# Performance work log

Measured on AMD Instinct MI355X. Metric: run time of the kernel, lower is better.

Reference implementation:

```python
import jax, jax.numpy as jnp
import numpy as np

B, S, D, E, K, NS = 4, 1024, 1024, 8, 2, 2
H = 4 * D
TEMP = 0.1
SCALE = 0.02


def setup_inputs() -> dict:
    key = jax.random.key(0)
    ks = jax.random.split(key, 12)
    f32 = jnp.float32
    return {
        "x": jax.random.normal(ks[0], (B, S, D), f32),
        "Ws1": jax.random.normal(ks[1], (NS, D, H), f32) * SCALE,
        "bs1": jnp.zeros((NS, H), f32),
        "Ws2": jax.random.normal(ks[2], (NS, H, D), f32) * SCALE,
        "bs2": jnp.zeros((NS, D), f32),
        "We1": jax.random.normal(ks[3], (E, D, H), f32) * SCALE,
        "be1": jnp.zeros((E, H), f32),
        "We2": jax.random.normal(ks[4], (E, H, D), f32) * SCALE,
        "be2": jnp.zeros((E, D), f32),
        "Wr": jax.random.normal(ks[5], (D, E), f32) * SCALE,
        "br": jnp.zeros((E,), f32),
        "gumbel": jax.random.gumbel(ks[6], (B, S, E), f32),
    }


def reference(x, Ws1, bs1, Ws2, bs2, We1, be1, We2, be2, Wr, br, gumbel):
    act = jax.nn.gelu
    # shared experts: dense FFN per shared expert, summed over experts
    hs = act(jnp.einsum('bsd,edh->ebsh', x, Ws1) + bs1[:, None, None, :])
    shared_sum = (jnp.einsum('ebsh,ehd->ebsd', hs, Ws2)
                  + bs2[:, None, None, :]).sum(axis=0)  # [B,S,D]
    # routing experts: ALL experts computed densely over all tokens
    he = act(jnp.einsum('bsd,edh->ebsh', x, We1) + be1[:, None, None, :])
    all_experts = jnp.einsum('ebsh,ehd->ebsd', he, We2) + be2[:, None, None, :]  # [E,B,S,D]
    # router + gumbel-softmax top-k selection
    logits = x @ Wr + br                                  # [B,S,E]
    router_probs = jax.nn.softmax((logits + gumbel) / TEMP, axis=-1)
    chosen = jax.lax.top_k(router_probs, K)[1]            # [B,S,K] int
    one_hot = jax.nn.one_hot(chosen, E, dtype=x.dtype)    # [B,S,K,E]
    # unweighted sum of selected experts' outputs (sum over k and experts)
    out = jnp.einsum('bske,ebsd->bsd', one_hot, all_experts)
    return out + shared_sum
```

## Files before the change

kernel.cpp:

```cpp
#include <hip/hip_runtime.h>
#include <cstdint>
#include <cstddef>

#define T_TOK 4096
#define DDIM 1024
#define HDIM 4096
#define NEXP 8
#define NSHARED 2
#define RT_CAP 9216

typedef unsigned short ushort_t;
typedef __attribute__((ext_vector_type(8))) short short8;
typedef __attribute__((ext_vector_type(4))) float f32x4;

__device__ inline ushort_t f2bf(float f) {
  unsigned u = __float_as_uint(f);
  u += 0x7fffu + ((u >> 16) & 1u);
  return (ushort_t)(u >> 16);
}

__device__ inline void async_copy16(const ushort_t* g, ushort_t* l) {
  __builtin_amdgcn_global_load_lds(
      (const __attribute__((address_space(1))) void*)g,
      (__attribute__((address_space(3))) void*)l, 16, 0, 0);
}

__device__ inline float gelu_tanh(float x) {
  float u = 0.7978845608028654f * (x + 0.044715f * x * x * x);
  float th = 1.0f - 2.0f / (__expf(2.0f * u) + 1.0f);
  return 0.5f * x * (1.0f + th);
}

__device__ inline void swizzle_xy(int* bx, int* by) {
  int l = blockIdx.x + gridDim.x * blockIdx.y;
  int g = l >> 8;
  *bx = (l & 7) + (g << 3);
  *by = (l >> 3) & 31;
}

__global__ __launch_bounds__(256) void router_kernel(
    const float* __restrict__ x, const float* __restrict__ Wr,
    const float* __restrict__ br, const float* __restrict__ gum,
    int* __restrict__ choice, int* __restrict__ cnt) {
  int lane = threadIdx.x & 63;
  int wv = blockIdx.x * 4 + (threadIdx.x >> 6);
  if (wv >= T_TOK) return;
  const float* xr = x + (long)wv * DDIM;
  float acc[NEXP] = {0.f, 0.f, 0.f, 0.f, 0.f, 0.f, 0.f, 0.f};
  for (int d = lane; d < DDIM; d += 64) {
    float xv = xr[d];
    const float* w = Wr + d * NEXP;
#pragma unroll
    for (int e = 0; e < NEXP; e++) acc[e] += xv * w[e];
  }
#pragma unroll
  for (int e = 0; e < NEXP; e++) {
    float v = acc[e];
#pragma unroll
    for (int o = 32; o > 0; o >>= 1) v += __shfl_down(v, o);
    acc[e] = v;
  }
  if (lane == 0) {
    float vals[NEXP];
#pragma unroll
    for (int e = 0; e < NEXP; e++) vals[e] = acc[e] + br[e] + gum[(long)wv * NEXP + e];
    int i1 = 0; float b1 = vals[0];
#pragma unroll
    for (int e = 1; e < NEXP; e++) if (vals[e] > b1) { b1 = vals[e]; i1 = e; }
    int i2 = -1; float b2 = -3.4e38f;
#pragma unroll
    for (int e = 0; e < NEXP; e++) if (e != i1 && vals[e] > b2) { b2 = vals[e]; i2 = e; }
    choice[wv] = i1 | (i2 << 4);
    atomicAdd(&cnt[i1], 1);
    atomicAdd(&cnt[i2], 1);
  }
}

__global__ void prefix_kernel(const int* __restrict__ cnt, int* __restrict__ base,
                              int* __restrict__ fill) {
  if (threadIdx.x == 0 && blockIdx.x == 0) {
    int off = 0;
    for (int e = 0; e < NEXP; e++) {
      base[e] = off;
      off += (cnt[e] + 127) & ~127;
      fill[e] = 0;
    }
  }
}

__global__ __launch_bounds__(256) void scatter_kernel(
    const int* __restrict__ choice, const int* __restrict__ base,
    int* __restrict__ fill, int* __restrict__ idx, int* __restrict__ pos) {
  int t = blockIdx.x * 256 + threadIdx.x;
  if (t >= T_TOK) return;
  int c = choice[t];
  int e1 = c & 15, e2 = (c >> 4) & 15;
  int p1 = base[e1] + atomicAdd(&fill[e1], 1);
  idx[p1] = t; pos[2 * t] = p1;
  int p2 = base[e2] + atomicAdd(&fill[e2], 1);
  idx[p2] = t; pos[2 * t + 1] = p2;
}

__global__ __launch_bounds__(256) void cast_x_kernel(
    const float* __restrict__ in, ushort_t* __restrict__ out, int n4) {
  int i = blockIdx.x * 256 + threadIdx.x;
  if (i >= n4) return;
  float4 v = ((const float4*)in)[i];
  ushort4 o = make_ushort4(f2bf(v.x), f2bf(v.y), f2bf(v.z), f2bf(v.w));
  ((ushort4*)out)[i] = o;
}

__global__ __launch_bounds__(256) void transpose_cast10(
    const float* __restrict__ inS, const float* __restrict__ inE,
    ushort_t* __restrict__ out, int R, int C) {
  __shared__ float tile[32][33];
  int z = blockIdx.z;
  const float* in = (z < NSHARED) ? inS + (size_t)z * R * C
                                  : inE + (size_t)(z - NSHARED) * R * C;
  ushort_t* op = out + (size_t)z * R * C;
  int c0 = blockIdx.x * 32, r0 = blockIdx.y * 32;
  int tx = threadIdx.x, ty = threadIdx.y;
#pragma unroll
  for (int k = 0; k < 4; k++)
    tile[ty + 8 * k][tx] = in[(long)(r0 + ty + 8 * k) * C + (c0 + tx)];
  __syncthreads();
#pragma unroll
  for (int k = 0; k < 4; k++)
    op[(long)(c0 + ty + 8 * k) * R + (r0 + tx)] = f2bf(tile[tx][ty + 8 * k]);
}

__global__ __launch_bounds__(256) void gemm1_kernel(
    const ushort_t* __restrict__ xb, const ushort_t* __restrict__ W1t,
    const float* __restrict__ bs1, const float* __restrict__ be1,
    ushort_t* __restrict__ h_sh, ushort_t* __restrict__ h_rt,
    const int* __restrict__ cnt, const int* __restrict__ base,
    const int* __restrict__ idx) {
  __shared__ ushort_t As[2 * 128 * 32];
  __shared__ ushort_t Bs[2 * 128 * 32];

  int tid = threadIdx.x;
  int z = blockIdx.z;
  int bx, by; swizzle_xy(&bx, &by);
  int row0 = by * 128, col0 = bx * 128;
  bool sh = (z < NSHARED);

  int e = 0, M = T_TOK, base_e = 0;
  const ushort_t* Bp;
  const float* bias;
  if (sh) {
    Bp = W1t + (size_t)z * HDIM * DDIM;
    bias = bs1 + (size_t)z * HDIM;
  } else {
    e = z - NSHARED; M = cnt[e];
    if (row0 >= M) return;
    base_e = base[e];
    Bp = W1t + (size_t)(NSHARED + e) * HDIM * DDIM;
    bias = be1 + (size_t)e * HDIM;
  }

  int tq = tid & 3, tr = tid >> 2;
  const ushort_t *aS, *aS2;
  if (sh) {
    aS = xb + (size_t)(row0 + tr) * DDIM + tq * 8;
    aS2 = aS + (size_t)64 * DDIM;
  } else {
    int s1 = row0 + tr;      if (s1 > M - 1) s1 = M - 1;
    int s2 = row0 + tr + 64; if (s2 > M - 1) s2 = M - 1;
    aS  = xb + (size_t)idx[base_e + s1] * DDIM + tq * 8;
    aS2 = xb + (size_t)idx[base_e + s2] * DDIM + tq * 8;
  }
  const ushort_t* bS = Bp + (size_t)(col0 + tr) * DDIM + tq * 8;
  const ushort_t* bS2 = bS + (size_t)64 * DDIM;
  ushort_t* aD = As + tid * 8;
  ushort_t* bD = Bs + tid * 8;

  int lane = tid & 63, wv = tid >> 6;
  int wr = wv >> 1, wc = wv & 1;
  int ln = lane & 15, quad = lane >> 4;
  f32x4 acc[4][4] = {};
  const ushort_t* aLds = As + (wr * 64 + ln) * 32 + quad * 8;
  const ushort_t* bLds = Bs + (wc * 64 + ln) * 32 + quad * 8;

  for (int k0 = 0; k0 < DDIM; k0 += 64) {
    async_copy16(aS, aD);             async_copy16(aS2, aD + 2048);
    async_copy16(aS + 32, aD + 4096); async_copy16(aS2 + 32, aD + 6144);
    async_copy16(bS, bD);             async_copy16(bS2, bD + 2048);
    async_copy16(bS + 32, bD + 4096); async_copy16(bS2 + 32, bD + 6144);
    __syncthreads();
#pragma unroll
    for (int s = 0; s < 2; s++) {
      short8 af[4], bf[4];
#pragma unroll
      for (int i = 0; i < 4; i++) {
        af[i] = *(const short8*)(aLds + s * 4096 + i * 16 * 32);
        bf[i] = *(const short8*)(bLds + s * 4096 + i * 16 * 32);
      }
#pragma unroll
      for (int i = 0; i < 4; i++)
#pragma unroll
        for (int j = 0; j < 4; j++)
          acc[i][j] = __builtin_amdgcn_mfma_f32_16x16x32_bf16(af[i], bf[j],
                                                              acc[i][j], 0, 0, 0);
    }
    __syncthreads();
    aS += 64; aS2 += 64; bS += 64; bS2 += 64;
  }

#pragma unroll
  for (int i = 0; i < 4; i++) {
    int rowB = row0 + wr * 64 + i * 16 + quad * 4;
#pragma unroll
    for (int j = 0; j < 4; j++) {
      int col = col0 + wc * 64 + j * 16 + ln;
      float b = bias[col];
#pragma unroll
      for (int r = 0; r < 4; r++) {
        int t = rowB + r;
        float v = gelu_tanh(acc[i][j][r] + b);
        if (sh) {
          h_sh[(size_t)t * (2 * HDIM) + (size_t)z * HDIM + col] = f2bf(v);
        } else if (t < M) {
          h_rt[((size_t)base_e + t) * HDIM + col] = f2bf(v);
        }
      }
    }
  }
}

__global__ __launch_bounds__(256) void gemm2_kernel(
    const ushort_t* __restrict__ h_sh, const ushort_t* __restrict__ h_rt,
    const ushort_t* __restrict__ W2t, float* __restrict__ outShA,
    float* __restrict__ outShB, float* __restrict__ outRt,
    const int* __restrict__ cnt, const int* __restrict__ base) {
  __shared__ ushort_t As[2 * 128 * 32];
  __shared__ ushort_t Bs[2 * 128 * 32];

  int tid = threadIdx.x;
  int z = blockIdx.z;
  int bx, by; swizzle_xy(&bx, &by);
  int row0 = by * 128, col0 = bx * 128;
  bool sh = (z < NSHARED);

  int e = 0, M = T_TOK, base_e = 0;
  const ushort_t* Ap;
  long lda;
  const ushort_t* Bp;
  float* outP;
  if (sh) {
    Ap = h_sh + (size_t)z * HDIM;
    lda = 2 * HDIM;
    Bp = W2t + (size_t)z * DDIM * HDIM;
    outP = (z == 0) ? outShA : outShB;
  } else {
    e = z - NSHARED; M = cnt[e];
    if (row0 >= M) return;
    base_e = base[e];
    Ap = h_rt + (size_t)base_e * HDIM;
    lda = HDIM;
    Bp = W2t + (size_t)(NSHARED + e) * DDIM * HDIM;
    outP = outRt + (size_t)base_e * DDIM;
  }

  int tq = tid & 3, tr = tid >> 2;
  const ushort_t* aS = Ap + (long)(row0 + tr) * lda + tq * 8;
  const ushort_t* aS2 = aS + 64L * lda;
  const ushort_t* bS = Bp + (size_t)(col0 + tr) * HDIM + tq * 8;
  const ushort_t* bS2 = bS + (size_t)64 * HDIM;
  ushort_t* aD = As + tid * 8;
  ushort_t* bD = Bs + tid * 8;

  int lane = tid & 63, wv = tid >> 6;
  int wr = wv >> 1, wc = wv & 1;
  int ln = lane & 15, quad = lane >> 4;
  f32x4 acc[4][4] = {};
  const ushort_t* aLds = As + (wr * 64 + ln) * 32 + quad * 8;
  const ushort_t* bLds = Bs + (wc * 64 + ln) * 32 + quad * 8;

  for (int k0 = 0; k0 < HDIM; k0 += 64) {
    async_copy16(aS, aD);             async_copy16(aS2, aD + 2048);
    async_copy16(aS + 32, aD + 4096); async_copy16(aS2 + 32, aD + 6144);
    async_copy16(bS, bD);             async_copy16(bS2, bD + 2048);
    async_copy16(bS + 32, bD + 4096); async_copy16(bS2 + 32, bD + 6144);
    __syncthreads();
#pragma unroll
    for (int s = 0; s < 2; s++) {
      short8 af[4], bf[4];
#pragma unroll
      for (int i = 0; i < 4; i++) {
        af[i] = *(const short8*)(aLds + s * 4096 + i * 16 * 32);
        bf[i] = *(const short8*)(bLds + s * 4096 + i * 16 * 32);
      }
#pragma unroll
      for (int i = 0; i < 4; i++)
#pragma unroll
        for (int j = 0; j < 4; j++)
          acc[i][j] = __builtin_amdgcn_mfma_f32_16x16x32_bf16(af[i], bf[j],
                                                              acc[i][j], 0, 0, 0);
    }
    __syncthreads();
    aS += 64; aS2 += 64; bS += 64; bS2 += 64;
  }

#pragma unroll
  for (int i = 0; i < 4; i++) {
    int rowB = row0 + wr * 64 + i * 16 + quad * 4;
#pragma unroll
    for (int j = 0; j < 4; j++) {
      int col = col0 + wc * 64 + j * 16 + ln;
#pragma unroll
      for (int r = 0; r < 4; r++) {
        int t = rowB + r;
        if (sh || t < M) outP[(size_t)t * DDIM + col] = acc[i][j][r];
      }
    }
  }
}

__global__ __launch_bounds__(256) void combine_kernel(
    const float* __restrict__ shA, const float* __restrict__ shB,
    const float* __restrict__ rt, const float* __restrict__ bs2,
    const float* __restrict__ be2, const int* __restrict__ choice,
    const int* __restrict__ pos, float* __restrict__ out) {
  int i = blockIdx.x * 256 + threadIdx.x;
  int t = i >> 8;
  int d4 = i & 255;
  int c = choice[t];
  int e1 = c & 15, e2 = (c >> 4) & 15;
  long p1 = (long)pos[2 * t] * 256 + d4;
  long p2 = (long)pos[2 * t + 1] * 256 + d4;
  float4 a = ((const float4*)shA)[i];
  float4 b = ((const float4*)shB)[i];
  float4 r1 = ((const float4*)rt)[p1];
  float4 r2 = ((const float4*)rt)[p2];
  float4 b0 = ((const float4*)bs2)[d4];
  float4 b1 = ((const float4*)bs2)[256 + d4];
  float4 c1 = ((const float4*)be2)[e1 * 256 + d4];
  float4 c2 = ((const float4*)be2)[e2 * 256 + d4];
  float4 o;
  o.x = a.x + b.x + r1.x + r2.x + b0.x + b1.x + c1.x + c2.x;
  o.y = a.y + b.y + r1.y + r2.y + b0.y + b1.y + c1.y + c2.y;
  o.z = a.z + b.z + r1.z + r2.z + b0.z + b1.z + c1.z + c2.z;
  o.w = a.w + b.w + r1.w + r2.w + b0.w + b1.w + c1.w + c2.w;
  ((float4*)out)[i] = o;
}

extern "C" void kernel_launch(void* const* d_in, const int* in_sizes, int n_in,
                              void* d_out, int out_size, void* d_ws,
                              size_t ws_size, hipStream_t stream) {
  const float* x   = (const float*)d_in[0];
  const float* Ws1 = (const float*)d_in[1];
  const float* bs1 = (const float*)d_in[2];
  const float* Ws2 = (const float*)d_in[3];
  const float* bs2 = (const float*)d_in[4];
  const float* We1 = (const float*)d_in[5];
  const float* be1 = (const float*)d_in[6];
  const float* We2 = (const float*)d_in[7];
  const float* be2 = (const float*)d_in[8];
  const float* Wr  = (const float*)d_in[9];
  const float* br  = (const float*)d_in[10];
  const float* gum = (const float*)d_in[11];
  float* out = (float*)d_out;

  char* ws = (char*)d_ws;
  size_t off = 0;
  int* cnt    = (int*)(ws + off); off += 256;
  int* base   = (int*)(ws + off); off += 256;
  int* fill   = (int*)(ws + off); off += 256;
  int* choice = (int*)(ws + off); off += T_TOK * 4;
  int* idx    = (int*)(ws + off); off += RT_CAP * 4;
  int* pos    = (int*)(ws + off); off += T_TOK * 8;
  off = (off + 255) & ~(size_t)255;
  ushort_t* xb   = (ushort_t*)(ws + off); off += (size_t)T_TOK * DDIM * 2;
  ushort_t* W1t  = (ushort_t*)(ws + off); off += (size_t)10 * HDIM * DDIM * 2;
  ushort_t* W2t  = (ushort_t*)(ws + off); off += (size_t)10 * DDIM * HDIM * 2;
  ushort_t* h_sh = (ushort_t*)(ws + off); off += (size_t)T_TOK * 2 * HDIM * 2;
  ushort_t* h_rt = (ushort_t*)(ws + off); off += (size_t)RT_CAP * HDIM * 2;
  float* outShA = (float*)W1t;
  float* outShB = outShA + (size_t)T_TOK * DDIM;
  float* outRt  = outShB + (size_t)T_TOK * DDIM;
  (void)ws_size;

  hipMemsetAsync(cnt, 0, 256, stream);
  router_kernel<<<T_TOK / 4, 256, 0, stream>>>(x, Wr, br, gum, choice, cnt);
  prefix_kernel<<<1, 64, 0, stream>>>(cnt, base, fill);
  scatter_kernel<<<T_TOK / 256, 256, 0, stream>>>(choice, base, fill, idx, pos);
  cast_x_kernel<<<(T_TOK * DDIM / 4 + 255) / 256, 256, 0, stream>>>(
      x, xb, T_TOK * DDIM / 4);

  transpose_cast10<<<dim3(HDIM / 32, DDIM / 32, 10), dim3(32, 8), 0, stream>>>(
      Ws1, We1, W1t, DDIM, HDIM);
  transpose_cast10<<<dim3(DDIM / 32, HDIM / 32, 10), dim3(32, 8), 0, stream>>>(
      Ws2, We2, W2t, HDIM, DDIM);

  gemm1_kernel<<<dim3(HDIM / 128, T_TOK / 128, NSHARED + NEXP), 256, 0, stream>>>(
      xb, W1t, bs1, be1, h_sh, h_rt, cnt, base, idx);
  gemm2_kernel<<<dim3(DDIM / 128, T_TOK / 128, NSHARED + NEXP), 256, 0, stream>>>(
      h_sh, h_rt, W2t, outShA, outShB, outRt, cnt, base);
  combine_kernel<<<T_TOK * DDIM / 4 / 256, 256, 0, stream>>>(
      outShA, outShB, outRt, bs2, be2, choice, pos, out);

  (void)in_sizes; (void)n_in; (void)out_size;
}
```

Before: 1.038 ms.

## Double-buffer LDS tiles in both expert GEMMs and simplify tanh-GELU

Result: slower. 1.160 ms (+11.7%).

```diff
diff --git a/kernel.cpp b/kernel.cpp
--- a/kernel.cpp
+++ b/kernel.cpp
@@ -26,9 +26,10 @@
 }
 
 __device__ inline float gelu_tanh(float x) {
-  float u = 0.7978845608028654f * (x + 0.044715f * x * x * x);
-  float th = 1.0f - 2.0f / (__expf(2.0f * u) + 1.0f);
-  return 0.5f * x * (1.0f + th);
+  float x2 = x * x;
+  float t = fmaf(0.07135481627133721f, x2, 1.5957691216057308f);
+  float e = __expf(-x * t);
+  return x * __builtin_amdgcn_rcpf(1.0f + e);
 }
 
 __device__ inline void swizzle_xy(int* bx, int* by) {
@@ -135,8 +136,8 @@
     ushort_t* __restrict__ h_sh, ushort_t* __restrict__ h_rt,
     const int* __restrict__ cnt, const int* __restrict__ base,
     const int* __restrict__ idx) {
-  __shared__ ushort_t As[2 * 128 * 32];
-  __shared__ ushort_t Bs[2 * 128 * 32];
+  __shared__ ushort_t As[2][8192];
+  __shared__ ushort_t Bs[2][8192];
 
   int tid = threadIdx.x;
   int z = blockIdx.z;
@@ -171,22 +172,39 @@
   }
   const ushort_t* bS = Bp + (size_t)(col0 + tr) * DDIM + tq * 8;
   const ushort_t* bS2 = bS + (size_t)64 * DDIM;
-  ushort_t* aD = As + tid * 8;
-  ushort_t* bD = Bs + tid * 8;
 
   int lane = tid & 63, wv = tid >> 6;
   int wr = wv >> 1, wc = wv & 1;
   int ln = lane & 15, quad = lane >> 4;
   f32x4 acc[4][4] = {};
-  const ushort_t* aLds = As + (wr * 64 + ln) * 32 + quad * 8;
-  const ushort_t* bLds = Bs + (wc * 64 + ln) * 32 + quad * 8;
-
-  for (int k0 = 0; k0 < DDIM; k0 += 64) {
+  int ldsOfsA = (wr * 64 + ln) * 32 + quad * 8;
+  int ldsOfsB = (wc * 64 + ln) * 32 + quad * 8;
+
+  {
+    ushort_t* aD = As[0] + tid * 8;
+    ushort_t* bD = Bs[0] + tid * 8;
     async_copy16(aS, aD);             async_copy16(aS2, aD + 2048);
     async_copy16(aS + 32, aD + 4096); async_copy16(aS2 + 32, aD + 6144);
     async_copy16(bS, bD);             async_copy16(bS2, bD + 2048);
     async_copy16(bS + 32, bD + 4096); async_copy16(bS2 + 32, bD + 6144);
-    __syncthreads();
+    aS += 64; aS2 += 64; bS += 64; bS2 += 64;
+  }
+  __syncthreads();
+
+  const int NT = DDIM / 64;
+  int cur = 0;
+  for (int t = 0; t < NT; ++t) {
+    if (t + 1 < NT) {
+      ushort_t* aD = As[cur ^ 1] + tid * 8;
+      ushort_t* bD = Bs[cur ^ 1] + tid * 8;
+      async_copy16(aS, aD);             async_copy16(aS2, aD + 2048);
+      async_copy16(aS + 32, aD + 4096); async_copy16(aS2 + 32, aD + 6144);
+      async_copy16(bS, bD);             async_copy16(bS2, bD + 2048);
+      async_copy16(bS + 32, bD + 4096); async_copy16(bS2 + 32, bD + 6144);
+      aS += 64; aS2 += 64; bS += 64; bS2 += 64;
+    }
+    const ushort_t* aLds = As[cur] + ldsOfsA;
+    const ushort_t* bLds = Bs[cur] + ldsOfsB;
 #pragma unroll
     for (int s = 0; s < 2; s++) {
       short8 af[4], bf[4];
@@ -203,7 +221,7 @@
                                                               acc[i][j], 0, 0, 0);
     }
     __syncthreads();
-    aS += 64; aS2 += 64; bS += 64; bS2 += 64;
+    cur ^= 1;
   }
 
 #pragma unroll
@@ -232,8 +250,8 @@
     const ushort_t* __restrict__ W2t, float* __restrict__ outShA,
     float* __restrict__ outShB, float* __restrict__ outRt,
     const int* __restrict__ cnt, const int* __restrict__ base) {
-  __shared__ ushort_t As[2 * 128 * 32];
-  __shared__ ushort_t Bs[2 * 128 * 32];
+  __shared__ ushort_t As[2][8192];
+  __shared__ ushort_t Bs[2][8192];
 
   int tid = threadIdx.x;
   int z = blockIdx.z;
@@ -266,22 +284,39 @@
   const ushort_t* aS2 = aS + 64L * lda;
   const ushort_t* bS = Bp + (size_t)(col0 + tr) * HDIM + tq * 8;
   const ushort_t* bS2 = bS + (size_t)64 * HDIM;
-  ushort_t* aD = As + tid * 8;
-  ushort_t* bD = Bs + tid * 8;
 
   int lane = tid & 63, wv = tid >> 6;
   int wr = wv >> 1, wc = wv & 1;
   int ln = lane & 15, quad = lane >> 4;
   f32x4 acc[4][4] = {};
-  const ushort_t* aLds = As + (wr * 64 + ln) * 32 + quad * 8;
-  const ushort_t* bLds = Bs + (wc * 64 + ln) * 32 + quad * 8;
-
-  for (int k0 = 0; k0 < HDIM; k0 += 64) {
+  int ldsOfsA = (wr * 64 + ln) * 32 + quad * 8;
+  int ldsOfsB = (wc * 64 + ln) * 32 + quad * 8;
+
+  {
+    ushort_t* aD = As[0] + tid * 8;
+    ushort_t* bD = Bs[0] + tid * 8;
     async_copy16(aS, aD);             async_copy16(aS2, aD + 2048);
     async_copy16(aS + 32, aD + 4096); async_copy16(aS2 + 32, aD + 6144);
     async_copy16(bS, bD);             async_copy16(bS2, bD + 2048);
     async_copy16(bS + 32, bD + 4096); async_copy16(bS2 + 32, bD + 6144);
-    __syncthreads();
+    aS += 64; aS2 += 64; bS += 64; bS2 += 64;
+  }
+  __syncthreads();
+
+  const int NT = HDIM / 64;
+  int cur = 0;
+  for (int t = 0; t < NT; ++t) {
+    if (t + 1 < NT) {
+      ushort_t* aD = As[cur ^ 1] + tid * 8;
+      ushort_t* bD = Bs[cur ^ 1] + tid * 8;
+      async_copy16(aS, aD);             async_copy16(aS2, aD + 2048);
+      async_copy16(aS + 32, aD + 4096); async_copy16(aS2 + 32, aD + 6144);
+      async_copy16(bS, bD);             async_copy16(bS2, bD + 2048);
+      async_copy16(bS + 32, bD + 4096); async_copy16(bS2 + 32, bD + 6144);
+      aS += 64; aS2 += 64; bS += 64; bS2 += 64;
+    }
+    const ushort_t* aLds = As[cur] + ldsOfsA;
+    const ushort_t* bLds = Bs[cur] + ldsOfsB;
 #pragma unroll
     for (int s = 0; s < 2; s++) {
       short8 af[4], bf[4];
@@ -298,7 +333,7 @@
                                                               acc[i][j], 0, 0, 0);
     }
     __syncthreads();
-    aS += 64; aS2 += 64; bS += 64; bS2 += 64;
+    cur ^= 1;
   }
 
 #pragma unroll
```

## Triple-buffer GEMM LDS tiles with async prefetch and single barrier per step

Applied to the files above, without the earlier changes.

Measured after the change: 1.111 ms. 1.07x slower.

```diff
diff --git a/kernel.cpp b/kernel.cpp
--- a/kernel.cpp
+++ b/kernel.cpp
@@ -26,9 +26,10 @@
 }
 
 __device__ inline float gelu_tanh(float x) {
-  float u = 0.7978845608028654f * (x + 0.044715f * x * x * x);
-  float th = 1.0f - 2.0f / (__expf(2.0f * u) + 1.0f);
-  return 0.5f * x * (1.0f + th);
+  float x2 = x * x;
+  float t = fmaf(0.07135481627133721f, x2, 1.5957691216057308f);
+  float e = __expf(-x * t);
+  return x * __builtin_amdgcn_rcpf(1.0f + e);
 }
 
 __device__ inline void swizzle_xy(int* bx, int* by) {
@@ -37,6 +38,13 @@
   *bx = (l & 7) + (g << 3);
   *by = (l >> 3) & 31;
 }
+
+#define PIPE_BOUNDARY()                                     \
+  __builtin_amdgcn_sched_barrier(0);                        \
+  asm volatile("s_waitcnt vmcnt(4)" ::: "memory");          \
+  __builtin_amdgcn_s_barrier();                             \
+  asm volatile("" ::: "memory");                            \
+  __builtin_amdgcn_sched_barrier(0);
 
 __global__ __launch_bounds__(256) void router_kernel(
     const float* __restrict__ x, const float* __restrict__ Wr,
@@ -135,8 +143,8 @@
     ushort_t* __restrict__ h_sh, ushort_t* __restrict__ h_rt,
     const int* __restrict__ cnt, const int* __restrict__ base,
     const int* __restrict__ idx) {
-  __shared__ ushort_t As[2 * 128 * 32];
-  __shared__ ushort_t Bs[2 * 128 * 32];
+  __shared__ ushort_t As[3][4096];
+  __shared__ ushort_t Bs[3][4096];
 
   int tid = threadIdx.x;
   int z = blockIdx.z;
@@ -159,52 +167,67 @@
   }
 
   int tq = tid & 3, tr = tid >> 2;
-  const ushort_t *aS, *aS2;
+  const ushort_t *aP0, *aP1;
   if (sh) {
-    aS = xb + (size_t)(row0 + tr) * DDIM + tq * 8;
-    aS2 = aS + (size_t)64 * DDIM;
+    aP0 = xb + (size_t)(row0 + tr) * DDIM + tq * 8;
+    aP1 = aP0 + (size_t)64 * DDIM;
   } else {
     int s1 = row0 + tr;      if (s1 > M - 1) s1 = M - 1;
     int s2 = row0 + tr + 64; if (s2 > M - 1) s2 = M - 1;
-    aS  = xb + (size_t)idx[base_e + s1] * DDIM + tq * 8;
-    aS2 = xb + (size_t)idx[base_e + s2] * DDIM + tq * 8;
-  }
-  const ushort_t* bS = Bp + (size_t)(col0 + tr) * DDIM + tq * 8;
-  const ushort_t* bS2 = bS + (size_t)64 * DDIM;
-  ushort_t* aD = As + tid * 8;
-  ushort_t* bD = Bs + tid * 8;
+    aP0 = xb + (size_t)idx[base_e + s1] * DDIM + tq * 8;
+    aP1 = xb + (size_t)idx[base_e + s2] * DDIM + tq * 8;
+  }
+  const ushort_t* bP0 = Bp + (size_t)(col0 + tr) * DDIM + tq * 8;
+  const ushort_t* bP1 = bP0 + (size_t)64 * DDIM;
 
   int lane = tid & 63, wv = tid >> 6;
   int wr = wv >> 1, wc = wv & 1;
   int ln = lane & 15, quad = lane >> 4;
   f32x4 acc[4][4] = {};
-  const ushort_t* aLds = As + (wr * 64 + ln) * 32 + quad * 8;
-  const ushort_t* bLds = Bs + (wc * 64 + ln) * 32 + quad * 8;
-
-  for (int k0 = 0; k0 < DDIM; k0 += 64) {
-    async_copy16(aS, aD);             async_copy16(aS2, aD + 2048);
-    async_copy16(aS + 32, aD + 4096); async_copy16(aS2 + 32, aD + 6144);
-    async_copy16(bS, bD);             async_copy16(bS2, bD + 2048);
-    async_copy16(bS + 32, bD + 4096); async_copy16(bS2 + 32, bD + 6144);
-    __syncthreads();
-#pragma unroll
-    for (int s = 0; s < 2; s++) {
-      short8 af[4], bf[4];
-#pragma unroll
-      for (int i = 0; i < 4; i++) {
-        af[i] = *(const short8*)(aLds + s * 4096 + i * 16 * 32);
-        bf[i] = *(const short8*)(bLds + s * 4096 + i * 16 * 32);
-      }
-#pragma unroll
-      for (int i = 0; i < 4; i++)
-#pragma unroll
-        for (int j = 0; j < 4; j++)
-          acc[i][j] = __builtin_amdgcn_mfma_f32_16x16x32_bf16(af[i], bf[j],
-                                                              acc[i][j], 0, 0, 0);
-    }
-    __syncthreads();
-    aS += 64; aS2 += 64; bS += 64; bS2 += 64;
-  }
+  const int ofsA = (wr * 64 + ln) * 32 + quad * 8;
+  const int ofsB = (wc * 64 + ln) * 32 + quad * 8;
+
+#define G1_STAGE(t, c)                                            \
+  {                                                               \
+    size_t kk = (size_t)(t) * 32;                                 \
+    async_copy16(aP0 + kk, As[c] + tid * 8);                      \
+    async_copy16(aP1 + kk, As[c] + tid * 8 + 2048);               \
+    async_copy16(bP0 + kk, Bs[c] + tid * 8);                      \
+    async_copy16(bP1 + kk, Bs[c] + tid * 8 + 2048);               \
+  }
+
+#define G1_COMPUTE(c)                                             \
+  {                                                               \
+    const ushort_t* aL = As[c] + ofsA;                            \
+    const ushort_t* bL = Bs[c] + ofsB;                            \
+    short8 af[4], bf[4];                                          \
+    _Pragma("unroll") for (int i = 0; i < 4; i++) {               \
+      af[i] = *(const short8*)(aL + i * 512);                     \
+      bf[i] = *(const short8*)(bL + i * 512);                     \
+    }                                                             \
+    __builtin_amdgcn_s_setprio(1);                                \
+    _Pragma("unroll") for (int i = 0; i < 4; i++)                 \
+      _Pragma("unroll") for (int j = 0; j < 4; j++)               \
+        acc[i][j] = __builtin_amdgcn_mfma_f32_16x16x32_bf16(      \
+            af[i], bf[j], acc[i][j], 0, 0, 0);                    \
+    __builtin_amdgcn_s_setprio(0);                                \
+  }
+
+  const int NT = DDIM / 32;
+  G1_STAGE(0, 0);
+  G1_STAGE(1, 1);
+  PIPE_BOUNDARY();
+
+  int c0 = 0, c1 = 1, c2 = 2;
+  for (int t = 0; t < NT - 2; ++t) {
+    G1_STAGE(t + 2, c2);
+    G1_COMPUTE(c0);
+    PIPE_BOUNDARY();
+    int tmp = c0; c0 = c1; c1 = c2; c2 = tmp;
+  }
+  G1_COMPUTE(c0);
+  __syncthreads();
+  G1_COMPUTE(c1);
 
 #pragma unroll
   for (int i = 0; i < 4; i++) {
@@ -225,6 +248,8 @@
       }
     }
   }
+#undef G1_STAGE
+#undef G1_COMPUTE
 }
 
 __global__ __launch_bounds__(256) void gemm2_kernel(
@@ -232,8 +257,8 @@
     const ushort_t* __restrict__ W2t, float* __restrict__ outShA,
     float* __restrict__ outShB, float* __restrict__ outRt,
     const int* __restrict__ cnt, const int* __restrict__ base) {
-  __shared__ ushort_t As[2 * 128 * 32];
-  __shared__ ushort_t Bs[2 * 128 * 32];
+  __shared__ ushort_t As[3][4096];
+  __shared__ ushort_t Bs[3][4096];
 
   int tid = threadIdx.x;
   int z = blockIdx.z;
@@ -262,44 +287,59 @@
   }
 
   int tq = tid & 3, tr = tid >> 2;
-  const ushort_t* aS = Ap + (long)(row0 + tr) * lda + tq * 8;
-  const ushort_t* aS2 = aS + 64L * lda;
-  const ushort_t* bS = Bp + (size_t)(col0 + tr) * HDIM + tq * 8;
-  const ushort_t* bS2 = bS + (size_t)64 * HDIM;
-  ushort_t* aD = As + tid * 8;
-  ushort_t* bD = Bs + tid * 8;
+  const ushort_t* aP0 = Ap + (long)(row0 + tr) * lda + tq * 8;
+  const ushort_t* aP1 = aP0 + 64L * lda;
+  const ushort_t* bP0 = Bp + (size_t)(col0 + tr) * HDIM + tq * 8;
+  const ushort_t* bP1 = bP0 + (size_t)64 * HDIM;
 
   int lane = tid & 63, wv = tid >> 6;
   int wr = wv >> 1, wc = wv & 1;
   int ln = lane & 15, quad = lane >> 4;
   f32x4 acc[4][4] = {};
-  const ushort_t* aLds = As + (wr * 64 + ln) * 32 + quad * 8;
-  const ushort_t* bLds = Bs + (wc * 64 + ln) * 32 + quad * 8;
-
-  for (int k0 = 0; k0 < HDIM; k0 += 64) {
-    async_copy16(aS, aD);             async_copy16(aS2, aD + 2048);
-    async_copy16(aS + 32, aD + 4096); async_copy16(aS2 + 32, aD + 6144);
-    async_copy16(bS, bD);             async_copy16(bS2, bD + 2048);
-    async_copy16(bS + 32, bD + 4096); async_copy16(bS2 + 32, bD + 6144);
-    __syncthreads();
-#pragma unroll
-    for (int s = 0; s < 2; s++) {
-      short8 af[4], bf[4];
-#pragma unroll
-      for (int i = 0; i < 4; i++) {
-        af[i] = *(const short8*)(aLds + s * 4096 + i * 16 * 32);
-        bf[i] = *(const short8*)(bLds + s * 4096 + i * 16 * 32);
-      }
-#pragma unroll
-      for (int i = 0; i < 4; i++)
-#pragma unroll
-        for (int j = 0; j < 4; j++)
-          acc[i][j] = __builtin_amdgcn_mfma_f32_16x16x32_bf16(af[i], bf[j],
-                                                              acc[i][j], 0, 0, 0);
-    }
-    __syncthreads();
-    aS += 64; aS2 += 64; bS += 64; bS2 += 64;
-  }
+  const int ofsA = (wr * 64 + ln) * 32 + quad * 8;
+  const int ofsB = (wc * 64 + ln) * 32 + quad * 8;
+
+#define G2_STAGE(t, c)                                            \
+  {                                                               \
+    size_t kk = (size_t)(t) * 32;                                 \
+    async_copy16(aP0 + kk, As[c] + tid * 8);                      \
+    async_copy16(aP1 + kk, As[c] + tid * 8 + 2048);               \
+    async_copy16(bP0 + kk, Bs[c] + tid * 8);                      \
+    async_copy16(bP1 + kk, Bs[c] + tid * 8 + 2048);               \
+  }
+
+#define G2_COMPUTE(c)                                             \
+  {                                                               \
+    const ushort_t* aL = As[c] + ofsA;                            \
+    const ushort_t* bL = Bs[c] + ofsB;                            \
+    short8 af[4], bf[4];                                          \
+    _Pragma("unroll") for (int i = 0; i < 4; i++) {               \
+      af[i] = *(const short8*)(aL + i * 512);                     \
+      bf[i] = *(const short8*)(bL + i * 512);                     \
+    }                                                             \
+    __builtin_amdgcn_s_setprio(1);                                \
+    _Pragma("unroll") for (int i = 0; i < 4; i++)                 \
+      _Pragma("unroll") for (int j = 0; j < 4; j++)               \
+        acc[i][j] = __builtin_amdgcn_mfma_f32_16x16x32_bf16(      \
+            af[i], bf[j], acc[i][j], 0, 0, 0);                    \
+    __builtin_amdgcn_s_setprio(0);                                \
+  }
+
+  const int NT = HDIM / 32;
+  G2_STAGE(0, 0);
+  G2_STAGE(1, 1);
+  PIPE_BOUNDARY();
+
+  int c0 = 0, c1 = 1, c2 = 2;
+  for (int t = 0; t < NT - 2; ++t) {
+    G2_STAGE(t + 2, c2);
+    G2_COMPUTE(c0);
+    PIPE_BOUNDARY();
+    int tmp = c0; c0 = c1; c1 = c2; c2 = tmp;
+  }
+  G2_COMPUTE(c0);
+  __syncthreads();
+  G2_COMPUTE(c1);
 
 #pragma unroll
   for (int i = 0; i < 4; i++) {
@@ -314,6 +354,8 @@
       }
     }
   }
+#undef G2_STAGE
+#undef G2_COMPUTE
 }
 
 __global__ __launch_bounds__(256) void combine_kernel(
```
